# Kernel tuning notes

Measured on AMD Instinct MI355X. Metric: run time of the kernel, lower is better.

Reference implementation:

```python
import jax, jax.numpy as jnp
import numpy as np

N = 50000
E = 800000
G = 2500  # number of graphs


def setup_inputs() -> dict:
    key = jax.random.key(0)
    ks = jax.random.split(key, 10)
    x = jax.random.normal(ks[0], (N, 128), dtype=jnp.float32)
    edge_index = jax.random.randint(ks[1], (2, E), 0, N, dtype=jnp.int64)
    batch = jnp.sort(jax.random.randint(ks[2], (N,), 0, G, dtype=jnp.int64))
    def lin(k, fan_in, shape):
        return jax.random.normal(k, shape, dtype=jnp.float32) / np.sqrt(fan_in)
    return {
        'x': x, 'edge_index': edge_index, 'batch': batch,
        'W1': lin(ks[3], 128, (128, 64)), 'b1': jnp.zeros((64,), jnp.float32),
        'W2': lin(ks[4], 64, (64, 64)),  'b2': jnp.zeros((64,), jnp.float32),
        'W3': lin(ks[5], 64, (64, 64)),  'b3': jnp.zeros((64,), jnp.float32),
        'Wp1': lin(ks[6], 64, (64, 64)), 'bp1': jnp.zeros((64,), jnp.float32),
        'Wp2': lin(ks[7], 64, (64, 32)), 'bp2': jnp.zeros((32,), jnp.float32),
    }


def _gcn_norm(edge_index, n_nodes):
    # PyG GCNConv default: add self-loops, symmetric normalization
    loops = jnp.arange(n_nodes, dtype=edge_index.dtype)
    src = jnp.concatenate([edge_index[0], loops])
    dst = jnp.concatenate([edge_index[1], loops])
    deg = jax.ops.segment_sum(jnp.ones_like(dst, dtype=jnp.float32), dst,
                              num_segments=n_nodes)
    dis = jnp.where(deg > 0, jax.lax.rsqrt(deg), 0.0)
    norm = dis[src] * dis[dst]  # [E + N]
    return src, dst, norm


def _gcn_conv(x, W, b, src, dst, norm, n_nodes):
    h = x @ W                                   # transform first (small dim)
    m = h[src] * norm[:, None]                  # gather + scale
    out = jax.ops.segment_sum(m, dst, num_segments=n_nodes)  # scatter-add
    return out + b


def reference(x, edge_index, batch, W1, b1, W2, b2, W3, b3, Wp1, bp1, Wp2, bp2):
    n_nodes = x.shape[0]
    src, dst, norm = _gcn_norm(edge_index, n_nodes)
    x1 = jax.nn.relu(_gcn_conv(x, W1, b1, src, dst, norm, n_nodes))
    x2 = jax.nn.relu(_gcn_conv(x1, W2, b2, src, dst, norm, n_nodes))
    x3 = jax.nn.relu(_gcn_conv(x2, W3, b3, src, dst, norm, n_nodes))
    h = x1 + x2 + x3
    # global_mean_pool
    sums = jax.ops.segment_sum(h, batch, num_segments=G)
    counts = jax.ops.segment_sum(jnp.ones((n_nodes,), jnp.float32), batch,
                                 num_segments=G)
    pooled = sums / jnp.maximum(counts, 1.0)[:, None]
    z = jax.nn.relu(pooled @ Wp1 + bp1) @ Wp2 + bp2
    return z
```

## Files before the change

### kernel.cpp

```cpp
#include <hip/hip_runtime.h>
#include <math.h>


typedef short short8 __attribute__((ext_vector_type(8)));
typedef float f32x4 __attribute__((ext_vector_type(4)));

__device__ inline float bf2f(unsigned short h) {
    return __uint_as_float((unsigned)h << 16);
}
__device__ inline unsigned short f2bf(float f) {
    unsigned u = __float_as_uint(f);
    return (unsigned short)((u + (0x7FFFu + ((u >> 16) & 1u))) >> 16);
}
__device__ inline unsigned short f2h(float f) {
    union { _Float16 h; unsigned short u; } c;
    c.h = (_Float16)f;
    return c.u;
}
__device__ inline float h2f(unsigned short u) {
    union { unsigned short u; _Float16 h; } c;
    c.u = u;
    return (float)c.h;
}
__device__ inline void bh8f(short8 u, float4& a, float4& b) {
    a.x = bf2f((unsigned short)u[0]); a.y = bf2f((unsigned short)u[1]);
    a.z = bf2f((unsigned short)u[2]); a.w = bf2f((unsigned short)u[3]);
    b.x = bf2f((unsigned short)u[4]); b.y = bf2f((unsigned short)u[5]);
    b.z = bf2f((unsigned short)u[6]); b.w = bf2f((unsigned short)u[7]);
}
__device__ inline float4 f4fma(float s, float4 a, float4 acc) {
    acc.x += s * a.x; acc.y += s * a.y; acc.z += s * a.z; acc.w += s * a.w;
    return acc;
}

__global__ void kA_hist(const int* __restrict__ dst, int* __restrict__ hist,
                        int E, int chunk) {
    __shared__ int h[256];
    int t = threadIdx.x;
    h[t] = 0;
    __syncthreads();
    int e0 = blockIdx.x * chunk;
    int e1 = min(e0 + chunk, E);
    for (int e = e0 + t; e < e1; e += 256) atomicAdd(&h[dst[e] >> 8], 1);
    __syncthreads();
    hist[blockIdx.x * 256 + t] = h[t];
}

__global__ void kA_colscan(const int* __restrict__ hist, int* __restrict__ cursorA,
                           int* __restrict__ tot) {
    __shared__ int s[256];
    int t = threadIdx.x;
    int k = blockIdx.x;
    int v = hist[t * 256 + k];
    s[t] = v;
    __syncthreads();
    for (int st = 1; st < 256; st <<= 1) {
        int u = s[t];
        if (t >= st) u += s[t - st];
        __syncthreads();
        s[t] = u;
        __syncthreads();
    }
    cursorA[t * 256 + k] = s[t] - v;
    if (t == 255) tot[k] = s[255];
}

__global__ void kA_scatter(const int* __restrict__ src, const int* __restrict__ dst,
                           const int* __restrict__ cursorA, const int* __restrict__ tot,
                           unsigned* __restrict__ ebuf, int E, int chunk) {
    __shared__ int s[256];
    __shared__ int cur[256];
    int t = threadIdx.x;
    s[t] = tot[t];
    __syncthreads();
    for (int st = 1; st < 256; st <<= 1) {
        int u = s[t];
        if (t >= st) u += s[t - st];
        __syncthreads();
        s[t] = u;
        __syncthreads();
    }
    int bstart = (t == 0) ? 0 : s[t - 1];
    cur[t] = cursorA[blockIdx.x * 256 + t] + bstart;
    __syncthreads();
    int e0 = blockIdx.x * chunk;
    int e1 = min(e0 + chunk, E);
    for (int e = e0 + t; e < e1; e += 256) {
        int d = dst[e];
        int p = atomicAdd(&cur[d >> 8], 1);
        ebuf[p] = ((unsigned)(d & 255) << 24) | (unsigned)src[e];
    }
}

__global__ void kB1(const unsigned* __restrict__ ebuf, const int* __restrict__ tot,
                    float* __restrict__ dis, int* __restrict__ offs, int N, int E) {
    __shared__ int s[256];
    __shared__ int h[256];
    int t = threadIdx.x;
    int k = blockIdx.x;
    s[t] = tot[t];
    __syncthreads();
    for (int st = 1; st < 256; st <<= 1) {
        int u = s[t];
        if (t >= st) u += s[t - st];
        __syncthreads();
        s[t] = u;
        __syncthreads();
    }
    int lo = (k == 0) ? 0 : s[k - 1];
    int hi = s[k];
    h[t] = 0;
    __syncthreads();
    for (int p = lo + t; p < hi; p += 256) atomicAdd(&h[ebuf[p] >> 24], 1);
    __syncthreads();
    int c = h[t];
    int node = k * 256 + t;
    if (node < N) dis[node] = rsqrtf((float)(c + 1));
    s[t] = c;
    __syncthreads();
    for (int st = 1; st < 256; st <<= 1) {
        int u = s[t];
        if (t >= st) u += s[t - st];
        __syncthreads();
        s[t] = u;
        __syncthreads();
    }
    if (node < N) offs[node] = lo + s[t] - c;
    if (node == N - 1) offs[N] = E;
}

__global__ void kB2(const unsigned* __restrict__ ebuf, const int* __restrict__ tot,
                    const float* __restrict__ dis, const int* __restrict__ offs,
                    unsigned* __restrict__ col, int N, int E) {
    __shared__ int s[256];
    __shared__ int cur[256];
    int t = threadIdx.x;
    int k = blockIdx.x;
    s[t] = tot[t];
    __syncthreads();
    for (int st = 1; st < 256; st <<= 1) {
        int u = s[t];
        if (t >= st) u += s[t - st];
        __syncthreads();
        s[t] = u;
        __syncthreads();
    }
    int lo = (k == 0) ? 0 : s[k - 1];
    int hi = s[k];
    int node = k * 256 + t;
    cur[t] = (node < N) ? offs[node] : 0;
    __syncthreads();
    for (int p = lo + t; p < hi; p += 256) {
        unsigned e = ebuf[p];
        int srcI = (int)(e & 0x00FFFFFFu);
        int q = atomicAdd(&cur[e >> 24], 1);
        col[q] = ((unsigned)f2h(dis[srcI]) << 16) | (unsigned)srcI;
    }
}

template <int K>
__global__ __launch_bounds__(256) void k_gemm_f32(const float* __restrict__ X,
                                                  const float* __restrict__ W,
                                                  unsigned short* __restrict__ H, int n) {
    __shared__ short wt[64 * K];
    int t = threadIdx.x;
    for (int idx = t; idx < 64 * K; idx += 256) {
        int k = idx >> 6, ch = idx & 63;
        wt[ch * K + k] = (short)f2bf(W[idx]);
    }
    __syncthreads();
    int wave = t >> 6, lane = t & 63;
    int q = lane >> 4, l = lane & 15;
    int tile = blockIdx.x * 4 + wave;
    if (tile * 16 >= n) return;
    int node = tile * 16 + l;
    short8 afr[4][K / 32];
#pragma unroll
    for (int mb = 0; mb < 4; mb++)
#pragma unroll
        for (int s = 0; s < K / 32; s++)
            afr[mb][s] = *(const short8*)(wt + (mb * 16 + l) * K + s * 32 + q * 8);
    f32x4 acc[4] = {};
    const float* xr = X + (size_t)node * K + q * 8;
#pragma unroll
    for (int s = 0; s < K / 32; s++) {
        float4 xa = *(const float4*)(xr + s * 32);
        float4 xb = *(const float4*)(xr + s * 32 + 4);
        short8 bfr;
        bfr[0] = (short)f2bf(xa.x); bfr[1] = (short)f2bf(xa.y);
        bfr[2] = (short)f2bf(xa.z); bfr[3] = (short)f2bf(xa.w);
        bfr[4] = (short)f2bf(xb.x); bfr[5] = (short)f2bf(xb.y);
        bfr[6] = (short)f2bf(xb.z); bfr[7] = (short)f2bf(xb.w);
#pragma unroll
        for (int mb = 0; mb < 4; mb++)
            acc[mb] = __builtin_amdgcn_mfma_f32_16x16x32_bf16(afr[mb][s], bfr, acc[mb], 0, 0, 0);
    }
#pragma unroll
    for (int mb = 0; mb < 4; mb++) {
        ushort4 u;
        u.x = f2bf(acc[mb][0]); u.y = f2bf(acc[mb][1]);
        u.z = f2bf(acc[mb][2]); u.w = f2bf(acc[mb][3]);
        ((ushort4*)H)[(size_t)node * 16 + mb * 4 + q] = u;
    }
}

__global__ __launch_bounds__(256) void k_aggemm(const unsigned short* __restrict__ H,
                                                const unsigned* __restrict__ col,
                                                const int* __restrict__ offs,
                                                const float* __restrict__ dis,
                                                const float* __restrict__ bias,
                                                const float* __restrict__ W,
                                                unsigned short* __restrict__ Xout,
                                                unsigned short* __restrict__ Hout, int n) {
    __shared__ short wt[64 * 64];
    __shared__ short vbuf[64 * 72];
    int t = threadIdx.x;
    for (int idx = t; idx < 64 * 64; idx += 256) {
        int k = idx >> 6, ch = idx & 63;
        wt[ch * 64 + k] = (short)f2bf(W[idx]);
    }
    const short8* Hs = (const short8*)H;
    int base = blockIdx.x * 64;
    int cs = t & 7;
    const float4* bias4 = (const float4*)bias;
    float4 bb0 = bias4[cs * 2];
    float4 bb1 = bias4[cs * 2 + 1];
#pragma unroll
    for (int r = 0; r < 2; r++) {
        int nl = r * 32 + (t >> 3);
        int node = base + nl;
        if (node < n) {
            float dn = dis[node];
            float4 acc0, acc1;
            bh8f(Hs[(size_t)node * 8 + cs], acc0, acc1);
            acc0.x *= dn; acc0.y *= dn; acc0.z *= dn; acc0.w *= dn;
            acc1.x *= dn; acc1.y *= dn; acc1.z *= dn; acc1.w *= dn;
            int lo = offs[node], hi = offs[node + 1];
            int p = lo;
            for (; p + 4 <= hi; p += 4) {
                unsigned e0 = col[p], e1 = col[p + 1], e2 = col[p + 2], e3 = col[p + 3];
                short8 g0 = Hs[(size_t)(e0 & 0xFFFFu) * 8 + cs];
                short8 g1 = Hs[(size_t)(e1 & 0xFFFFu) * 8 + cs];
                short8 g2 = Hs[(size_t)(e2 & 0xFFFFu) * 8 + cs];
                short8 g3 = Hs[(size_t)(e3 & 0xFFFFu) * 8 + cs];
                float w0 = h2f((unsigned short)(e0 >> 16));
                float w1 = h2f((unsigned short)(e1 >> 16));
                float w2 = h2f((unsigned short)(e2 >> 16));
                float w3 = h2f((unsigned short)(e3 >> 16));
                float4 a, b;
                bh8f(g0, a, b); acc0 = f4fma(w0, a, acc0); acc1 = f4fma(w0, b, acc1);
                bh8f(g1, a, b); acc0 = f4fma(w1, a, acc0); acc1 = f4fma(w1, b, acc1);
                bh8f(g2, a, b); acc0 = f4fma(w2, a, acc0); acc1 = f4fma(w2, b, acc1);
                bh8f(g3, a, b); acc0 = f4fma(w3, a, acc0); acc1 = f4fma(w3, b, acc1);
            }
            for (; p < hi; p++) {
                unsigned e = col[p];
                float w = h2f((unsigned short)(e >> 16));
                float4 a, b;
                bh8f(Hs[(size_t)(e & 0xFFFFu) * 8 + cs], a, b);
                acc0 = f4fma(w, a, acc0);
                acc1 = f4fma(w, b, acc1);
            }
            float4 v0, v1;
            v0.x = fmaxf(acc0.x * dn + bb0.x, 0.f);
            v0.y = fmaxf(acc0.y * dn + bb0.y, 0.f);
            v0.z = fmaxf(acc0.z * dn + bb0.z, 0.f);
            v0.w = fmaxf(acc0.w * dn + bb0.w, 0.f);
            v1.x = fmaxf(acc1.x * dn + bb1.x, 0.f);
            v1.y = fmaxf(acc1.y * dn + bb1.y, 0.f);
            v1.z = fmaxf(acc1.z * dn + bb1.z, 0.f);
            v1.w = fmaxf(acc1.w * dn + bb1.w, 0.f);
            short8 o;
            o[0] = (short)f2bf(v0.x); o[1] = (short)f2bf(v0.y);
            o[2] = (short)f2bf(v0.z); o[3] = (short)f2bf(v0.w);
            o[4] = (short)f2bf(v1.x); o[5] = (short)f2bf(v1.y);
            o[6] = (short)f2bf(v1.z); o[7] = (short)f2bf(v1.w);
            ((short8*)Xout)[(size_t)node * 8 + cs] = o;
            *(short8*)(vbuf + nl * 72 + cs * 8) = o;
        }
    }
    __syncthreads();
    int wave = t >> 6, lane = t & 63;
    int q = lane >> 4, l = lane & 15;
    if (base + wave * 16 >= n) return;
    int node = base + wave * 16 + l;
    short8 afr[4][2];
#pragma unroll
    for (int mb = 0; mb < 4; mb++)
#pragma unroll
        for (int s = 0; s < 2; s++)
            afr[mb][s] = *(const short8*)(wt + (mb * 16 + l) * 64 + s * 32 + q * 8);
    f32x4 acc[4] = {};
#pragma unroll
    for (int s = 0; s < 2; s++) {
        short8 bfr = *(const short8*)(vbuf + (wave * 16 + l) * 72 + s * 32 + q * 8);
#pragma unroll
        for (int mb = 0; mb < 4; mb++)
            acc[mb] = __builtin_amdgcn_mfma_f32_16x16x32_bf16(afr[mb][s], bfr, acc[mb], 0, 0, 0);
    }
#pragma unroll
    for (int mb = 0; mb < 4; mb++) {
        ushort4 u;
        u.x = f2bf(acc[mb][0]); u.y = f2bf(acc[mb][1]);
        u.z = f2bf(acc[mb][2]); u.w = f2bf(acc[mb][3]);
        ((ushort4*)Hout)[(size_t)node * 16 + mb * 4 + q] = u;
    }
}

__global__ void k_agg3(const unsigned short* __restrict__ H, const unsigned* __restrict__ col,
                       const int* __restrict__ offs, const float* __restrict__ dis,
                       const float* __restrict__ bias,
                       const unsigned short* __restrict__ add1,
                       const unsigned short* __restrict__ add2,
                       float* __restrict__ OutS, int n) {
    int t = threadIdx.x;
    int node = blockIdx.x * 32 + (t >> 3);
    if (node >= n) return;
    int lane = t & 7;
    const short8* Hs = (const short8*)H;
    float dn = dis[node];
    float4 acc0, acc1;
    bh8f(Hs[(size_t)node * 8 + lane], acc0, acc1);
    acc0.x *= dn; acc0.y *= dn; acc0.z *= dn; acc0.w *= dn;
    acc1.x *= dn; acc1.y *= dn; acc1.z *= dn; acc1.w *= dn;
    int lo = offs[node], hi = offs[node + 1];
    int p = lo;
    for (; p + 4 <= hi; p += 4) {
        unsigned e0 = col[p], e1 = col[p + 1], e2 = col[p + 2], e3 = col[p + 3];
        short8 g0 = Hs[(size_t)(e0 & 0xFFFFu) * 8 + lane];
        short8 g1 = Hs[(size_t)(e1 & 0xFFFFu) * 8 + lane];
        short8 g2 = Hs[(size_t)(e2 & 0xFFFFu) * 8 + lane];
        short8 g3 = Hs[(size_t)(e3 & 0xFFFFu) * 8 + lane];
        float w0 = h2f((unsigned short)(e0 >> 16));
        float w1 = h2f((unsigned short)(e1 >> 16));
        float w2 = h2f((unsigned short)(e2 >> 16));
        float w3 = h2f((unsigned short)(e3 >> 16));
        float4 a, b;
        bh8f(g0, a, b); acc0 = f4fma(w0, a, acc0); acc1 = f4fma(w0, b, acc1);
        bh8f(g1, a, b); acc0 = f4fma(w1, a, acc0); acc1 = f4fma(w1, b, acc1);
        bh8f(g2, a, b); acc0 = f4fma(w2, a, acc0); acc1 = f4fma(w2, b, acc1);
        bh8f(g3, a, b); acc0 = f4fma(w3, a, acc0); acc1 = f4fma(w3, b, acc1);
    }
    for (; p < hi; p++) {
        unsigned e = col[p];
        float w = h2f((unsigned short)(e >> 16));
        float4 a, b;
        bh8f(Hs[(size_t)(e & 0xFFFFu) * 8 + lane], a, b);
        acc0 = f4fma(w, a, acc0);
        acc1 = f4fma(w, b, acc1);
    }
    const float4* bias4 = (const float4*)bias;
    float4 bb0 = bias4[lane * 2];
    float4 bb1 = bias4[lane * 2 + 1];
    float4 v0, v1;
    v0.x = fmaxf(acc0.x * dn + bb0.x, 0.f);
    v0.y = fmaxf(acc0.y * dn + bb0.y, 0.f);
    v0.z = fmaxf(acc0.z * dn + bb0.z, 0.f);
    v0.w = fmaxf(acc0.w * dn + bb0.w, 0.f);
    v1.x = fmaxf(acc1.x * dn + bb1.x, 0.f);
    v1.y = fmaxf(acc1.y * dn + bb1.y, 0.f);
    v1.z = fmaxf(acc1.z * dn + bb1.z, 0.f);
    v1.w = fmaxf(acc1.w * dn + bb1.w, 0.f);
    size_t slot = (size_t)node * 8 + lane;
    float4 a10, a11, a20, a21;
    bh8f(((const short8*)add1)[slot], a10, a11);
    bh8f(((const short8*)add2)[slot], a20, a21);
    v0.x += a10.x + a20.x; v0.y += a10.y + a20.y;
    v0.z += a10.z + a20.z; v0.w += a10.w + a20.w;
    v1.x += a11.x + a21.x; v1.y += a11.y + a21.y;
    v1.z += a11.z + a21.z; v1.w += a11.w + a21.w;
    float4* S4 = (float4*)OutS;
    size_t oi = (size_t)node * 16 + (size_t)lane * 2;
    S4[oi] = v0;
    S4[oi + 1] = v1;
}

__global__ void k_poolhead(const float* __restrict__ S, const int* __restrict__ batch,
                           const float* __restrict__ Wp1, const float* __restrict__ bp1,
                           const float* __restrict__ Wp2, const float* __restrict__ bp2,
                           float* __restrict__ out, int n, int G) {
    int g = blockIdx.x;
    int j = threadIdx.x;
    int a = 0, b = n;
    while (a < b) { int m = (a + b) >> 1; if (batch[m] < g) a = m + 1; else b = m; }
    int beg = a;
    b = n;
    while (a < b) { int m = (a + b) >> 1; if (batch[m] < g + 1) a = m + 1; else b = m; }
    int end = a;
    float sum = 0.f;
    int i = beg;
    for (; i + 2 <= end; i += 2)
        sum += S[(size_t)i * 64 + j] + S[(size_t)(i + 1) * 64 + j];
    if (i < end) sum += S[(size_t)i * 64 + j];
    float cnt = (float)(end - beg);
    float p = sum / fmaxf(cnt, 1.f);
    __shared__ float ps[64];
    __shared__ float ts[64];
    ps[j] = p;
    __syncthreads();
    float t1 = bp1[j];
#pragma unroll 8
    for (int k = 0; k < 64; k++) t1 += ps[k] * Wp1[k * 64 + j];
    t1 = fmaxf(t1, 0.f);
    ts[j] = t1;
    __syncthreads();
    if (j < 32) {
        float o = bp2[j];
#pragma unroll 8
        for (int k = 0; k < 64; k++) o += ts[k] * Wp2[k * 32 + j];
        out[(size_t)g * 32 + j] = o;
    }
}

extern "C" void kernel_launch(void* const* d_in, const int* in_sizes, int n_in,
                              void* d_out, int out_size, void* d_ws, size_t ws_size,
                              hipStream_t stream) {
    const float* x   = (const float*)d_in[0];
    const int*   ei  = (const int*)d_in[1];
    const int*   bat = (const int*)d_in[2];
    const float* W1  = (const float*)d_in[3];
    const float* b1  = (const float*)d_in[4];
    const float* W2  = (const float*)d_in[5];
    const float* b2  = (const float*)d_in[6];
    const float* W3  = (const float*)d_in[7];
    const float* b3  = (const float*)d_in[8];
    const float* Wp1 = (const float*)d_in[9];
    const float* bp1 = (const float*)d_in[10];
    const float* Wp2 = (const float*)d_in[11];
    const float* bp2 = (const float*)d_in[12];

    int N = in_sizes[0] / 128;
    int E = in_sizes[1] / 2;
    int G = out_size / 32;
    const int* src = ei;
    const int* dst = ei + E;

    char* w = (char*)d_ws;
    auto alloc = [&](size_t bytes) -> void* {
        void* p = (void*)w;
        w += (bytes + 255) & ~(size_t)255;
        return p;
    };
    int NB = (N + 255) / 256;
    int*            offs    = (int*)alloc((size_t)(N + 1) * 4);
    unsigned*       col     = (unsigned*)alloc((size_t)E * 4);
    float*          dis     = (float*)alloc((size_t)N * 4);
    int*            hist    = (int*)alloc((size_t)256 * 256 * 4);
    int*            cursorA = (int*)alloc((size_t)256 * 256 * 4);
    int*            tot     = (int*)alloc((size_t)256 * 4);
    unsigned*       ebuf    = (unsigned*)alloc((size_t)E * 4);
    unsigned short* Hb      = (unsigned short*)alloc((size_t)N * 64 * 2);
    unsigned short* Hb2     = (unsigned short*)alloc((size_t)N * 64 * 2);
    unsigned short* X1      = (unsigned short*)alloc((size_t)N * 64 * 2);
    unsigned short* X2      = (unsigned short*)alloc((size_t)N * 64 * 2);
    float*          S       = (float*)alloc((size_t)N * 64 * 4);

    int chunk = (E + 255) / 256;

    kA_hist<<<256, 256, 0, stream>>>(dst, hist, E, chunk);
    kA_colscan<<<256, 256, 0, stream>>>(hist, cursorA, tot);
    kA_scatter<<<256, 256, 0, stream>>>(src, dst, cursorA, tot, ebuf, E, chunk);
    kB1<<<NB, 256, 0, stream>>>(ebuf, tot, dis, offs, N, E);
    kB2<<<NB, 256, 0, stream>>>(ebuf, tot, dis, offs, col, N, E);

    int ggemm = ((N >> 4) + 3) / 4;
    int gfuse = (N + 63) / 64;
    int gagg  = (N + 31) / 32;
    k_gemm_f32<128><<<ggemm, 256, 0, stream>>>(x, W1, Hb, N);
    k_aggemm<<<gfuse, 256, 0, stream>>>(Hb, col, offs, dis, b1, W2, X1, Hb2, N);
    k_aggemm<<<gfuse, 256, 0, stream>>>(Hb2, col, offs, dis, b2, W3, X2, Hb, N);
    k_agg3<<<gagg, 256, 0, stream>>>(Hb, col, offs, dis, b3, X1, X2, S, N);

    k_poolhead<<<G, 64, 0, stream>>>(S, bat, Wp1, bp1, Wp2, bp2, (float*)d_out, N, G);
}
```

Before: 227.1 us.

## Pad CSR rows to multiples of four and fuse histogram into first GEMM

Each node's neighbour list is padded to a multiple of four entries, with zero-weight filler, and stored at aligned offsets. Offset and count are packed into one int per node, so the aggregation loops can load four edges at once with a uint4 and drop the scalar tail loop. The destination histogram pass also runs as extra blocks inside the first-layer GEMM launch, which removes one kernel launch and lets the two overlap. The cost is extra col storage and memory traffic for the padding. The packed format limits a row to 511 padded entries and the padded offset to 22 bits.

```diff
diff --git a/kernel.cpp b/kernel.cpp
--- a/kernel.cpp
+++ b/kernel.cpp
@@ -33,137 +33,25 @@
     return acc;
 }
 
-__global__ void kA_hist(const int* __restrict__ dst, int* __restrict__ hist,
-                        int E, int chunk) {
-    __shared__ int h[256];
-    int t = threadIdx.x;
-    h[t] = 0;
-    __syncthreads();
-    int e0 = blockIdx.x * chunk;
-    int e1 = min(e0 + chunk, E);
-    for (int e = e0 + t; e < e1; e += 256) atomicAdd(&h[dst[e] >> 8], 1);
-    __syncthreads();
-    hist[blockIdx.x * 256 + t] = h[t];
-}
-
-__global__ void kA_colscan(const int* __restrict__ hist, int* __restrict__ cursorA,
-                           int* __restrict__ tot) {
-    __shared__ int s[256];
-    int t = threadIdx.x;
-    int k = blockIdx.x;
-    int v = hist[t * 256 + k];
-    s[t] = v;
-    __syncthreads();
-    for (int st = 1; st < 256; st <<= 1) {
-        int u = s[t];
-        if (t >= st) u += s[t - st];
-        __syncthreads();
-        s[t] = u;
-        __syncthreads();
-    }
-    cursorA[t * 256 + k] = s[t] - v;
-    if (t == 255) tot[k] = s[255];
-}
-
-__global__ void kA_scatter(const int* __restrict__ src, const int* __restrict__ dst,
-                           const int* __restrict__ cursorA, const int* __restrict__ tot,
-                           unsigned* __restrict__ ebuf, int E, int chunk) {
-    __shared__ int s[256];
-    __shared__ int cur[256];
-    int t = threadIdx.x;
-    s[t] = tot[t];
-    __syncthreads();
-    for (int st = 1; st < 256; st <<= 1) {
-        int u = s[t];
-        if (t >= st) u += s[t - st];
-        __syncthreads();
-        s[t] = u;
-        __syncthreads();
-    }
-    int bstart = (t == 0) ? 0 : s[t - 1];
-    cur[t] = cursorA[blockIdx.x * 256 + t] + bstart;
-    __syncthreads();
-    int e0 = blockIdx.x * chunk;
-    int e1 = min(e0 + chunk, E);
-    for (int e = e0 + t; e < e1; e += 256) {
-        int d = dst[e];
-        int p = atomicAdd(&cur[d >> 8], 1);
-        ebuf[p] = ((unsigned)(d & 255) << 24) | (unsigned)src[e];
-    }
-}
-
-__global__ void kB1(const unsigned* __restrict__ ebuf, const int* __restrict__ tot,
-                    float* __restrict__ dis, int* __restrict__ offs, int N, int E) {
-    __shared__ int s[256];
-    __shared__ int h[256];
-    int t = threadIdx.x;
-    int k = blockIdx.x;
-    s[t] = tot[t];
-    __syncthreads();
-    for (int st = 1; st < 256; st <<= 1) {
-        int u = s[t];
-        if (t >= st) u += s[t - st];
-        __syncthreads();
-        s[t] = u;
-        __syncthreads();
-    }
-    int lo = (k == 0) ? 0 : s[k - 1];
-    int hi = s[k];
-    h[t] = 0;
-    __syncthreads();
-    for (int p = lo + t; p < hi; p += 256) atomicAdd(&h[ebuf[p] >> 24], 1);
-    __syncthreads();
-    int c = h[t];
-    int node = k * 256 + t;
-    if (node < N) dis[node] = rsqrtf((float)(c + 1));
-    s[t] = c;
-    __syncthreads();
-    for (int st = 1; st < 256; st <<= 1) {
-        int u = s[t];
-        if (t >= st) u += s[t - st];
-        __syncthreads();
-        s[t] = u;
-        __syncthreads();
-    }
-    if (node < N) offs[node] = lo + s[t] - c;
-    if (node == N - 1) offs[N] = E;
-}
-
-__global__ void kB2(const unsigned* __restrict__ ebuf, const int* __restrict__ tot,
-                    const float* __restrict__ dis, const int* __restrict__ offs,
-                    unsigned* __restrict__ col, int N, int E) {
-    __shared__ int s[256];
-    __shared__ int cur[256];
-    int t = threadIdx.x;
-    int k = blockIdx.x;
-    s[t] = tot[t];
-    __syncthreads();
-    for (int st = 1; st < 256; st <<= 1) {
-        int u = s[t];
-        if (t >= st) u += s[t - st];
-        __syncthreads();
-        s[t] = u;
-        __syncthreads();
-    }
-    int lo = (k == 0) ? 0 : s[k - 1];
-    int hi = s[k];
-    int node = k * 256 + t;
-    cur[t] = (node < N) ? offs[node] : 0;
-    __syncthreads();
-    for (int p = lo + t; p < hi; p += 256) {
-        unsigned e = ebuf[p];
-        int srcI = (int)(e & 0x00FFFFFFu);
-        int q = atomicAdd(&cur[e >> 24], 1);
-        col[q] = ((unsigned)f2h(dis[srcI]) << 16) | (unsigned)srcI;
-    }
-}
-
 template <int K>
-__global__ __launch_bounds__(256) void k_gemm_f32(const float* __restrict__ X,
-                                                  const float* __restrict__ W,
-                                                  unsigned short* __restrict__ H, int n) {
+__global__ __launch_bounds__(256) void k_hist_gemm(const int* __restrict__ dst,
+                                                   int* __restrict__ hist, int E, int chunk,
+                                                   const float* __restrict__ X,
+                                                   const float* __restrict__ W,
+                                                   unsigned short* __restrict__ H, int n) {
+    __shared__ int hh[256];
     __shared__ short wt[64 * K];
     int t = threadIdx.x;
+    if (blockIdx.x < 256) {
+        hh[t] = 0;
+        __syncthreads();
+        int e0 = blockIdx.x * chunk;
+        int e1 = min(e0 + chunk, E);
+        for (int e = e0 + t; e < e1; e += 256) atomicAdd(&hh[dst[e] >> 8], 1);
+        __syncthreads();
+        hist[blockIdx.x * 256 + t] = hh[t];
+        return;
+    }
     for (int idx = t; idx < 64 * K; idx += 256) {
         int k = idx >> 6, ch = idx & 63;
         wt[ch * K + k] = (short)f2bf(W[idx]);
@@ -171,7 +59,7 @@
     __syncthreads();
     int wave = t >> 6, lane = t & 63;
     int q = lane >> 4, l = lane & 15;
-    int tile = blockIdx.x * 4 + wave;
+    int tile = (blockIdx.x - 256) * 4 + wave;
     if (tile * 16 >= n) return;
     int node = tile * 16 + l;
     short8 afr[4][K / 32];
@@ -204,9 +92,128 @@
     }
 }
 
+__global__ void kA_colscan(const int* __restrict__ hist, int* __restrict__ cursorA,
+                           int* __restrict__ tot) {
+    __shared__ int s[256];
+    int t = threadIdx.x;
+    int k = blockIdx.x;
+    int v = hist[t * 256 + k];
+    s[t] = v;
+    __syncthreads();
+    for (int st = 1; st < 256; st <<= 1) {
+        int u = s[t];
+        if (t >= st) u += s[t - st];
+        __syncthreads();
+        s[t] = u;
+        __syncthreads();
+    }
+    cursorA[t * 256 + k] = s[t] - v;
+    if (t == 255) tot[k] = s[255];
+}
+
+__global__ void kA_scatter(const int* __restrict__ src, const int* __restrict__ dst,
+                           const int* __restrict__ cursorA, const int* __restrict__ tot,
+                           unsigned* __restrict__ ebuf, int E, int chunk) {
+    __shared__ int s[256];
+    __shared__ int cur[256];
+    int t = threadIdx.x;
+    s[t] = tot[t];
+    __syncthreads();
+    for (int st = 1; st < 256; st <<= 1) {
+        int u = s[t];
+        if (t >= st) u += s[t - st];
+        __syncthreads();
+        s[t] = u;
+        __syncthreads();
+    }
+    int bstart = (t == 0) ? 0 : s[t - 1];
+    cur[t] = cursorA[blockIdx.x * 256 + t] + bstart;
+    __syncthreads();
+    int e0 = blockIdx.x * chunk;
+    int e1 = min(e0 + chunk, E);
+    for (int e = e0 + t; e < e1; e += 256) {
+        int d = dst[e];
+        int p = atomicAdd(&cur[d >> 8], 1);
+        ebuf[p] = ((unsigned)(d & 255) << 24) | (unsigned)src[e];
+    }
+}
+
+__global__ void kB1(const unsigned* __restrict__ ebuf, const int* __restrict__ tot,
+                    float* __restrict__ dis, int* __restrict__ offsP, int N) {
+    __shared__ int s[256];
+    __shared__ int h[256];
+    int t = threadIdx.x;
+    int k = blockIdx.x;
+    s[t] = tot[t];
+    __syncthreads();
+    for (int st = 1; st < 256; st <<= 1) {
+        int u = s[t];
+        if (t >= st) u += s[t - st];
+        __syncthreads();
+        s[t] = u;
+        __syncthreads();
+    }
+    int lo = (k == 0) ? 0 : s[k - 1];
+    int hi = s[k];
+    int padbase = lo + 768 * k;
+    h[t] = 0;
+    __syncthreads();
+    for (int p = lo + t; p < hi; p += 256) atomicAdd(&h[ebuf[p] >> 24], 1);
+    __syncthreads();
+    int c = h[t];
+    int cp = (c + 3) & ~3;
+    int node = k * 256 + t;
+    if (node < N) dis[node] = rsqrtf((float)(c + 1));
+    s[t] = cp;
+    __syncthreads();
+    for (int st = 1; st < 256; st <<= 1) {
+        int u = s[t];
+        if (t >= st) u += s[t - st];
+        __syncthreads();
+        s[t] = u;
+        __syncthreads();
+    }
+    if (node < N) offsP[node] = ((padbase + s[t] - cp) << 9) | cp;
+}
+
+__global__ void kB2(const unsigned* __restrict__ ebuf, const int* __restrict__ tot,
+                    const float* __restrict__ dis, const int* __restrict__ offsP,
+                    unsigned* __restrict__ col, int N) {
+    __shared__ int s[256];
+    __shared__ int cur[256];
+    int t = threadIdx.x;
+    int k = blockIdx.x;
+    s[t] = tot[t];
+    __syncthreads();
+    for (int st = 1; st < 256; st <<= 1) {
+        int u = s[t];
+        if (t >= st) u += s[t - st];
+        __syncthreads();
+        s[t] = u;
+        __syncthreads();
+    }
+    int lo = (k == 0) ? 0 : s[k - 1];
+    int hi = s[k];
+    int node = k * 256 + t;
+    int po = (node < N) ? offsP[node] : 0;
+    cur[t] = po >> 9;
+    __syncthreads();
+    for (int p = lo + t; p < hi; p += 256) {
+        unsigned e = ebuf[p];
+        int srcI = (int)(e & 0x00FFFFFFu);
+        int q = atomicAdd(&cur[e >> 24], 1);
+        col[q] = ((unsigned)f2h(dis[srcI]) << 16) | (unsigned)srcI;
+    }
+    __syncthreads();
+    if (node < N) {
+        int end = (po >> 9) + (po & 511);
+        for (int q = cur[t]; q < end; q++) col[q] = 0u;
+    }
+}
+
 __global__ __launch_bounds__(256) void k_aggemm(const unsigned short* __restrict__ H,
                                                 const unsigned* __restrict__ col,
-                                                const int* __restrict__ offs,
+                                                const int* __restrict__ offsP,
                                                 const float* __restrict__ dis,
                                                 const float* __restrict__ bias,
                                                 const float* __restrict__ W,
@@ -235,31 +242,23 @@
             bh8f(Hs[(size_t)node * 8 + cs], acc0, acc1);
             acc0.x *= dn; acc0.y *= dn; acc0.z *= dn; acc0.w *= dn;
             acc1.x *= dn; acc1.y *= dn; acc1.z *= dn; acc1.w *= dn;
-            int lo = offs[node], hi = offs[node + 1];
-            int p = lo;
-            for (; p + 4 <= hi; p += 4) {
-                unsigned e0 = col[p], e1 = col[p + 1], e2 = col[p + 2], e3 = col[p + 3];
-                short8 g0 = Hs[(size_t)(e0 & 0xFFFFu) * 8 + cs];
-                short8 g1 = Hs[(size_t)(e1 & 0xFFFFu) * 8 + cs];
-                short8 g2 = Hs[(size_t)(e2 & 0xFFFFu) * 8 + cs];
-                short8 g3 = Hs[(size_t)(e3 & 0xFFFFu) * 8 + cs];
-                float w0 = h2f((unsigned short)(e0 >> 16));
-                float w1 = h2f((unsigned short)(e1 >> 16));
-                float w2 = h2f((unsigned short)(e2 >> 16));
-                float w3 = h2f((unsigned short)(e3 >> 16));
+            int po = offsP[node];
+            int p = po >> 9, hi = p + (po & 511);
+            for (; p < hi; p += 4) {
+                uint4 e4 = *(const uint4*)(col + p);
+                short8 g0 = Hs[(size_t)(e4.x & 0xFFFFu) * 8 + cs];
+                short8 g1 = Hs[(size_t)(e4.y & 0xFFFFu) * 8 + cs];
+                short8 g2 = Hs[(size_t)(e4.z & 0xFFFFu) * 8 + cs];
+                short8 g3 = Hs[(size_t)(e4.w & 0xFFFFu) * 8 + cs];
+                float w0 = h2f((unsigned short)(e4.x >> 16));
+                float w1 = h2f((unsigned short)(e4.y >> 16));
+                float w2 = h2f((unsigned short)(e4.z >> 16));
+                float w3 = h2f((unsigned short)(e4.w >> 16));
                 float4 a, b;
                 bh8f(g0, a, b); acc0 = f4fma(w0, a, acc0); acc1 = f4fma(w0, b, acc1);
                 bh8f(g1, a, b); acc0 = f4fma(w1, a, acc0); acc1 = f4fma(w1, b, acc1);
                 bh8f(g2, a, b); acc0 = f4fma(w2, a, acc0); acc1 = f4fma(w2, b, acc1);
                 bh8f(g3, a, b); acc0 = f4fma(w3, a, acc0); acc1 = f4fma(w3, b, acc1);
-            }
-            for (; p < hi; p++) {
-                unsigned e = col[p];
-                float w = h2f((unsigned short)(e >> 16));
-                float4 a, b;
-                bh8f(Hs[(size_t)(e & 0xFFFFu) * 8 + cs], a, b);
-                acc0 = f4fma(w, a, acc0);
-                acc1 = f4fma(w, b, acc1);
             }
             float4 v0, v1;
             v0.x = fmaxf(acc0.x * dn + bb0.x, 0.f);
@@ -308,7 +307,7 @@
 }
 
 __global__ void k_agg3(const unsigned short* __restrict__ H, const unsigned* __restrict__ col,
-                       const int* __restrict__ offs, const float* __restrict__ dis,
+                       const int* __restrict__ offsP, const float* __restrict__ dis,
                        const float* __restrict__ bias,
                        const unsigned short* __restrict__ add1,
                        const unsigned short* __restrict__ add2,
@@ -323,31 +322,23 @@
     bh8f(Hs[(size_t)node * 8 + lane], acc0, acc1);
     acc0.x *= dn; acc0.y *= dn; acc0.z *= dn; acc0.w *= dn;
     acc1.x *= dn; acc1.y *= dn; acc1.z *= dn; acc1.w *= dn;
-    int lo = offs[node], hi = offs[node + 1];
-    int p = lo;
-    for (; p + 4 <= hi; p += 4) {
-        unsigned e0 = col[p], e1 = col[p + 1], e2 = col[p + 2], e3 = col[p + 3];
-        short8 g0 = Hs[(size_t)(e0 & 0xFFFFu) * 8 + lane];
-        short8 g1 = Hs[(size_t)(e1 & 0xFFFFu) * 8 + lane];
-        short8 g2 = Hs[(size_t)(e2 & 0xFFFFu) * 8 + lane];
-        short8 g3 = Hs[(size_t)(e3 & 0xFFFFu) * 8 + lane];
-        float w0 = h2f((unsigned short)(e0 >> 16));
-        float w1 = h2f((unsigned short)(e1 >> 16));
-        float w2 = h2f((unsigned short)(e2 >> 16));
-        float w3 = h2f((unsigned short)(e3 >> 16));
+    int po = offsP[node];
+    int p = po >> 9, hi = p + (po & 511);
+    for (; p < hi; p += 4) {
+        uint4 e4 = *(const uint4*)(col + p);
+        short8 g0 = Hs[(size_t)(e4.x & 0xFFFFu) * 8 + lane];
+        short8 g1 = Hs[(size_t)(e4.y & 0xFFFFu) * 8 + lane];
+        short8 g2 = Hs[(size_t)(e4.z & 0xFFFFu) * 8 + lane];
+        short8 g3 = Hs[(size_t)(e4.w & 0xFFFFu) * 8 + lane];
+        float w0 = h2f((unsigned short)(e4.x >> 16));
+        float w1 = h2f((unsigned short)(e4.y >> 16));
+        float w2 = h2f((unsigned short)(e4.z >> 16));
+        float w3 = h2f((unsigned short)(e4.w >> 16));
         float4 a, b;
         bh8f(g0, a, b); acc0 = f4fma(w0, a, acc0); acc1 = f4fma(w0, b, acc1);
         bh8f(g1, a, b); acc0 = f4fma(w1, a, acc0); acc1 = f4fma(w1, b, acc1);
         bh8f(g2, a, b); acc0 = f4fma(w2, a, acc0); acc1 = f4fma(w2, b, acc1);
         bh8f(g3, a, b); acc0 = f4fma(w3, a, acc0); acc1 = f4fma(w3, b, acc1);
-    }
-    for (; p < hi; p++) {
-        unsigned e = col[p];
-        float w = h2f((unsigned short)(e >> 16));
-        float4 a, b;
-        bh8f(Hs[(size_t)(e & 0xFFFFu) * 8 + lane], a, b);
-        acc0 = f4fma(w, a, acc0);
-        acc1 = f4fma(w, b, acc1);
     }
     const float4* bias4 = (const float4*)bias;
     float4 bb0 = bias4[lane * 2];
@@ -442,8 +433,8 @@
         return p;
     };
     int NB = (N + 255) / 256;
-    int*            offs    = (int*)alloc((size_t)(N + 1) * 4);
-    unsigned*       col     = (unsigned*)alloc((size_t)E * 4);
+    int*            offsP   = (int*)alloc((size_t)N * 4);
+    unsigned*       col     = (unsigned*)alloc(((size_t)E + 3 * (size_t)N + 1024) * 4);
     float*          dis     = (float*)alloc((size_t)N * 4);
     int*            hist    = (int*)alloc((size_t)256 * 256 * 4);
     int*            cursorA = (int*)alloc((size_t)256 * 256 * 4);
@@ -456,20 +447,19 @@
     float*          S       = (float*)alloc((size_t)N * 64 * 4);
 
     int chunk = (E + 255) / 256;
-
-    kA_hist<<<256, 256, 0, stream>>>(dst, hist, E, chunk);
-    kA_colscan<<<256, 256, 0, stream>>>(hist, cursorA, tot);
-    kA_scatter<<<256, 256, 0, stream>>>(src, dst, cursorA, tot, ebuf, E, chunk);
-    kB1<<<NB, 256, 0, stream>>>(ebuf, tot, dis, offs, N, E);
-    kB2<<<NB, 256, 0, stream>>>(ebuf, tot, dis, offs, col, N, E);
-
     int ggemm = ((N >> 4) + 3) / 4;
     int gfuse = (N + 63) / 64;
     int gagg  = (N + 31) / 32;
-    k_gemm_f32<128><<<ggemm, 256, 0, stream>>>(x, W1, Hb, N);
-    k_aggemm<<<gfuse, 256, 0, stream>>>(Hb, col, offs, dis, b1, W2, X1, Hb2, N);
-    k_aggemm<<<gfuse, 256, 0, stream>>>(Hb2, col, offs, dis, b2, W3, X2, Hb, N);
-    k_agg3<<<gagg, 256, 0, stream>>>(Hb, col, offs, dis, b3, X1, X2, S, N);
+
+    k_hist_gemm<128><<<256 + ggemm, 256, 0, stream>>>(dst, hist, E, chunk, x, W1, Hb, N);
+    kA_colscan<<<256, 256, 0, stream>>>(hist, cursorA, tot);
+    kA_scatter<<<256, 256, 0, stream>>>(src, dst, cursorA, tot, ebuf, E, chunk);
+    kB1<<<NB, 256, 0, stream>>>(ebuf, tot, dis, offsP, N);
+    kB2<<<NB, 256, 0, stream>>>(ebuf, tot, dis, offsP, col, N);
+
+    k_aggemm<<<gfuse, 256, 0, stream>>>(Hb, col, offsP, dis, b1, W2, X1, Hb2, N);
+    k_aggemm<<<gfuse, 256, 0, stream>>>(Hb2, col, offsP, dis, b2, W3, X2, Hb, N);
+    k_agg3<<<gagg, 256, 0, stream>>>(Hb, col, offsP, dis, b3, X1, X2, S, N);
 
     k_poolhead<<<G, 64, 0, stream>>>(S, bat, Wp1, bp1, Wp2, bp2, (float*)d_out, N, G);
 }
```

New measurement: 218.6 us (median of 2 runs). -3.7%, faster.
